# Kernel tuning notes

Measured on AMD Instinct MI355X. Metric: run time of the kernel, lower is better.

Reference implementation:

```python
import jax, jax.numpy as jnp
import numpy as np

B, NQ, NP = 4, 8192, 2048
DIM_INP, DIM, HID, OUT, NBLK = 256, 200, 128, 3, 5
VAR = 0.2 ** 2


def setup_inputs() -> dict:
    key = jax.random.key(0)
    ks = jax.random.split(key, 12)
    s = 0.05  # weight scale to keep activations sane
    return {
        "xyz_q": jax.random.uniform(ks[0], (B, NQ, 3), jnp.float32),
        "anchors": jax.random.uniform(ks[1], (B, NP, 3), jnp.float32),
        "anchor_feats": jax.random.normal(ks[2], (B, NP, DIM_INP), jnp.float32),
        "fc0_w": jax.random.normal(ks[3], (DIM_INP, DIM), jnp.float32) * s,
        "fc0_b": jnp.zeros((DIM,), jnp.float32),
        "fc1_w": jax.random.normal(ks[4], (DIM, HID), jnp.float32) * s,
        "fc1_b": jnp.zeros((HID,), jnp.float32),
        "blk_w0": jax.random.normal(ks[5], (NBLK, HID, HID), jnp.float32) * s,
        "blk_b0": jnp.zeros((NBLK, HID), jnp.float32),
        "blk_w1": jax.random.normal(ks[6], (NBLK, HID, HID), jnp.float32) * s,
        "blk_b1": jnp.zeros((NBLK, HID), jnp.float32),
        "fcc_w": jax.random.normal(ks[7], (NBLK, DIM, HID), jnp.float32) * s,
        "fcc_b": jnp.zeros((NBLK, HID), jnp.float32),
        "out_w": jax.random.normal(ks[8], (HID, OUT), jnp.float32) * s,
        "out_b": jnp.zeros((OUT,), jnp.float32),
    }


def reference(xyz_q, anchors, anchor_feats, fc0_w, fc0_b, fc1_w, fc1_b,
              blk_w0, blk_b0, blk_w1, blk_b1, fcc_w, fcc_b, out_w, out_b):
    relu = jax.nn.relu
    # Gaussian-kernel interpolation of anchor features at query points.
    # diff: [B, nq, np, 3]
    diff = anchors[:, None, :, :] - xyz_q[:, :, None, :]
    d = jnp.linalg.norm(diff, axis=-1)                    # [B, nq, np]
    logits = -((d + 1e-5) ** 2) / VAR
    weight = jax.nn.softmax(logits, axis=2)               # exp / sum, stable
    c = jnp.einsum('bqp,bpd->bqd', weight, anchor_feats)  # [B, nq, dim_inp]
    lat = c @ fc0_w + fc0_b                               # [B, nq, dim]
    net = relu(lat) @ fc1_w + fc1_b                       # [B, nq, hid]
    for i in range(NBLK):
        net = net + lat @ fcc_w[i] + fcc_b[i]
        # ResnetBlockFC: x + fc_1(relu(fc_0(relu(x))))
        dx = relu(relu(net) @ blk_w0[i] + blk_b0[i]) @ blk_w1[i] + blk_b1[i]
        net = net + dx
    return relu(net) @ out_w + out_b                      # [B, nq, 3]
```

## Files before the change

### kernel.cpp

```cpp
#include <hip/hip_runtime.h>
#include <math.h>

#define NP     2048
#define NQTOT  8192
#define DIN    256
#define DIM    200
#define HID    128
#define NOUT3  3
#define NBLK   5
#define TQ     32
#define NTHR   256
#define INVVAR 25.0f
#define NKT    (NP / 32)
#define NDT    (DIN / 16)
#define WSCALE 32768.0f
#define NFRAG  760

using f16x8 = __attribute__((ext_vector_type(8))) _Float16;
using f32x4 = __attribute__((ext_vector_type(4))) float;

__device__ __forceinline__ unsigned int pkrtz_u32(float a, float b) {
  auto p = __builtin_amdgcn_cvt_pkrtz(a, b);
  return __builtin_bit_cast(unsigned int, p);
}
__device__ __forceinline__ void pack_f16_2(const float* f, f16x8& h, f16x8& l) {
#pragma unroll
  for (int j = 0; j < 8; ++j) {
    const float v = f[j];
    const _Float16 hh = (_Float16)v;
    h[j] = hh; l[j] = (_Float16)(v - (float)hh);
  }
}
__device__ __forceinline__ void pack_w16(const float* f, f16x8& h, f16x8& l) {
#pragma unroll
  for (int j = 0; j < 8; ++j) {
    const float v = f[j] * WSCALE;
    const _Float16 hh = (_Float16)v;
    h[j] = hh; l[j] = (_Float16)(v - (float)hh);
  }
}
__device__ __forceinline__ void pack_a(const float* f, f16x8& h, f16x8& l) {
  union { f16x8 v; unsigned int u[4]; } H, L;
#pragma unroll
  for (int jp = 0; jp < 4; ++jp) {
    const float a = f[2 * jp], b = f[2 * jp + 1];
    auto hp = __builtin_amdgcn_cvt_pkrtz(a, b);
    H.u[jp] = __builtin_bit_cast(unsigned int, hp);
    L.u[jp] = pkrtz_u32(a - (float)hp[0], b - (float)hp[1]);
  }
  h = H.v; l = L.v;
}
__device__ __forceinline__ unsigned int split_pack(float x) {
  auto hp = __builtin_amdgcn_cvt_pkrtz(x, x);
  return pkrtz_u32(x, x - (float)hp[0]);
}

__device__ __forceinline__ int qsw(int r, int q) {
  return r * TQ + (q ^ (((r >> 2) & 7) << 2));
}
template<int KPAD>
__device__ __forceinline__ int sidx(int q, int k) {
  return q * KPAD + (((k >> 2) ^ (q & 7)) << 2) + (k & 3);
}

template<int KPAD, bool RELU>
__device__ __forceinline__ void store_split4(unsigned int* dst, int k, int qbase, f32x4 v) {
#pragma unroll
  for (int r = 0; r < 4; ++r) {
    float x = v[r];
    if (RELU) x = fmaxf(x, 0.f);
    dst[sidx<KPAD>(qbase + r, k)] = split_pack(x);
  }
}

__global__ __launch_bounds__(NTHR) void pid_packf(const float* __restrict__ F,
                                                  f16x8* __restrict__ wsHi,
                                                  f16x8* __restrict__ wsLo) {
  const int wid = threadIdx.x >> 6, l = threadIdx.x & 63;
  const int tile = blockIdx.x * 4 + wid;
  const int b  = tile >> 10;
  const int kt = (tile >> 4) & 63;
  const int dt = tile & 15;
  const int grp = l >> 4, qn = l & 15;
  const float* src = F + ((size_t)b * NP + kt * 32 + grp * 8) * DIN + dt * 16 + qn;
  float v[8];
#pragma unroll
  for (int j = 0; j < 8; ++j) v[j] = src[(size_t)j * DIN];
  f16x8 h, lo;
  pack_f16_2(v, h, lo);
  const size_t fi = (size_t)tile * 64 + l;
  wsHi[fi] = h; wsLo[fi] = lo;
}

__global__ __launch_bounds__(NTHR) void pid_packw(
    const float* __restrict__ fc0_w, const float* __restrict__ fc1_w,
    const float* __restrict__ fcc_w, const float* __restrict__ blk_w0,
    const float* __restrict__ blk_w1,
    f16x8* __restrict__ Wh, f16x8* __restrict__ Wm) {
  const int wid = threadIdx.x >> 6, l = threadIdx.x & 63;
  const int f = blockIdx.x * 4 + wid;
  if (f >= NFRAG) return;
  const float* src; int Kl, Nl, ks, nt;
  if (f < 104)      { int r = f;       src = fc0_w; Kl = 256; Nl = 200; ks = r / 13; nt = r % 13; }
  else if (f < 160) { int r = f - 104; src = fc1_w; Kl = 200; Nl = 128; ks = r / 8;  nt = r % 8; }
  else if (f < 440) { int r = f - 160; int i = r / 56; r %= 56;
                      src = fcc_w + (size_t)i * DIM * HID; Kl = 200; Nl = 128; ks = r / 8; nt = r % 8; }
  else if (f < 600) { int r = f - 440; int i = r / 32; r %= 32;
                      src = blk_w0 + (size_t)i * HID * HID; Kl = 128; Nl = 128; ks = r / 8; nt = r % 8; }
  else              { int r = f - 600; int i = r / 32; r %= 32;
                      src = blk_w1 + (size_t)i * HID * HID; Kl = 128; Nl = 128; ks = r / 8; nt = r % 8; }
  const int grp = l >> 4, n = nt * 16 + (l & 15);
  f16x8 h, m;
#pragma unroll
  for (int j = 0; j < 8; ++j) {
    const int k = ks * 32 + grp * 8 + j;
    const float v = (k < Kl && n < Nl) ? src[(size_t)k * Nl + n] : 0.f;
    const _Float16 hh = (_Float16)v;
    h[j] = hh; m[j] = (_Float16)(v - (float)hh);
  }
  const size_t fi = (size_t)f * 64 + l;
  Wh[fi] = h; Wm[fi] = m;
}

template<int KS, int NT, int MAXNT, int KPADIN, bool RELUA>
__device__ __forceinline__ void mm_stage(
    const unsigned int* __restrict__ Xs,
    const f16x8* __restrict__ Wh, const f16x8* __restrict__ Wm, int fbase,
    f32x4 acc[2][MAXNT], int wid, int l) {
  const int grp = l >> 4, qn = l & 15;
#pragma unroll 1
  for (int ks = 0; ks < KS; ++ks) {
    f16x8 bh[MAXNT], bm[MAXNT];
#pragma unroll
    for (int i = 0; i < MAXNT; ++i) {
      const int nt = wid + i * 4;
      if (nt < NT) {
        const size_t fi = (size_t)(fbase + ks * NT + nt) * 64 + l;
        bh[i] = Wh[fi]; bm[i] = Wm[fi];
      }
    }
    const int u0 = ks * 8 + grp * 2;
    f16x8 ah[2], al[2];
#pragma unroll
    for (int qt = 0; qt < 2; ++qt) {
      const int q = qt * 16 + qn;
      const unsigned int* row = Xs + q * KPADIN;
      const uint4 lo = *(const uint4*)(row + (((u0) ^ (q & 7)) << 2));
      const uint4 hi = *(const uint4*)(row + (((u0 + 1) ^ (q & 7)) << 2));
      unsigned int p[8] = {lo.x, lo.y, lo.z, lo.w, hi.x, hi.y, hi.z, hi.w};
      if (RELUA) {
#pragma unroll
        for (int j = 0; j < 8; ++j) p[j] = (p[j] & 0x8000u) ? 0u : p[j];
      }
      union { f16x8 v; unsigned int u[4]; } H, L;
#pragma unroll
      for (int jp = 0; jp < 4; ++jp) {
        H.u[jp] = __builtin_amdgcn_perm(p[2 * jp + 1], p[2 * jp], 0x05040100u);
        L.u[jp] = __builtin_amdgcn_perm(p[2 * jp + 1], p[2 * jp], 0x07060302u);
      }
      ah[qt] = H.v; al[qt] = L.v;
    }
#pragma unroll
    for (int qt = 0; qt < 2; ++qt)
#pragma unroll
      for (int i = 0; i < MAXNT; ++i)
        if (wid + i * 4 < NT) {
          acc[qt][i] = __builtin_amdgcn_mfma_f32_16x16x32_f16(ah[qt], bh[i], acc[qt][i], 0, 0, 0);
          acc[qt][i] = __builtin_amdgcn_mfma_f32_16x16x32_f16(ah[qt], bm[i], acc[qt][i], 0, 0, 0);
          acc[qt][i] = __builtin_amdgcn_mfma_f32_16x16x32_f16(al[qt], bh[i], acc[qt][i], 0, 0, 0);
        }
  }
}

struct SMemV2 {
  union {
    struct { float ax[NP * 3]; float qx[TQ], qy[TQ], qz[TQ]; } a;
    unsigned int lats[32 * 224];
  } r1;
  union {
    unsigned int cTs[32 * 256];
    struct { unsigned int nets[32 * 128]; unsigned int tmps[32 * 128]; } nt;
    float netf[128 * 32];
  } r2;
  float sS[64];
};

__global__ __launch_bounds__(NTHR, 2) void pid_fused_mfma(
    const float* __restrict__ xyz_q, const float* __restrict__ anchors,
    const f16x8* __restrict__ wsFh, const f16x8* __restrict__ wsFl,
    const f16x8* __restrict__ Wh, const f16x8* __restrict__ Wm,
    const float* __restrict__ fc0_b, const float* __restrict__ fc1_b,
    const float* __restrict__ blk_b0, const float* __restrict__ blk_b1,
    const float* __restrict__ fcc_b,
    const float* __restrict__ out_w, const float* __restrict__ out_b,
    float* __restrict__ out) {
  __shared__ SMemV2 sm;
  const int t = threadIdx.x;
  const int bi = blockIdx.x;
  const int batch = bi & 3;
  const int q0 = (bi >> 2) * TQ;

  {
    const float4* src = (const float4*)(anchors + (size_t)batch * NP * 3);
    float4* dst = (float4*)sm.r1.a.ax;
#pragma unroll
    for (int j = 0; j < (NP * 3 / 4) / NTHR; ++j)
      dst[j * NTHR + t] = src[j * NTHR + t];
  }
  if (t < TQ) {
    const float* qp = xyz_q + ((size_t)batch * NQTOT + q0 + t) * 3;
    sm.r1.a.qx[t] = qp[0]; sm.r1.a.qy[t] = qp[1]; sm.r1.a.qz[t] = qp[2];
  }
  __syncthreads();

  const int wid = t >> 6, l = t & 63;
  const int qt = wid & 1;
  const int kh = wid >> 1;
  const int grp = l >> 4, qn = l & 15;
  const float qxv = sm.r1.a.qx[qt * 16 + qn];
  const float qyv = sm.r1.a.qy[qt * 16 + qn];
  const float qzv = sm.r1.a.qz[qt * 16 + qn];
  const float nC1 = -36.067376f;
  const float nC2 = -7.2134752e-4f;

  const size_t fb0 = (size_t)batch * (NKT * NDT * 64) + (size_t)(kh * 32) * (NDT * 64) + l;
  const f16x8* pH0 = wsFh + fb0;        const f16x8* pL0 = wsFl + fb0;
  const f16x8* pH1 = pH0 + 256;         const f16x8* pL1 = pL0 + 256;
  const f16x8* pH2 = pH0 + 512;         const f16x8* pL2 = pL0 + 512;
  const f16x8* pH3 = pH0 + 768;         const f16x8* pL3 = pL0 + 768;

  f32x4 acc[16];
#pragma unroll
  for (int j = 0; j < 16; ++j) acc[j] = (f32x4){0.f, 0.f, 0.f, 0.f};
  float ssum = 0.f;

#pragma unroll 1
  for (int kt = 0; kt < 32; ++kt) {
    const int pb = (kh * 32 + kt) * 32 + grp * 8;
    float4 av[6];
    {
      const float4* ap = (const float4*)&sm.r1.a.ax[pb * 3];
#pragma unroll
      for (int j = 0; j < 6; ++j) av[j] = ap[j];
    }
    const float* af = (const float*)av;
    float w8[8];
#pragma unroll
    for (int j = 0; j < 8; ++j) {
      const float dx = af[3 * j] - qxv, dy = af[3 * j + 1] - qyv, dz = af[3 * j + 2] - qzv;
      const float D = fmaf(dx, dx, fmaf(dy, dy, dz * dz));
      const float s = __builtin_amdgcn_sqrtf(D);
      const float arg = fmaf(nC2, s, fmaf(nC1, D, 15.0f));
      const float u = __builtin_amdgcn_exp2f(arg);
      w8[j] = u; ssum += u;
    }
    f16x8 ah, al;
    pack_a(w8, ah, al);
#define CHUNK(dc, PH, PL)                                                     \
    {                                                                         \
      f16x8 bh[4], bl[4];                                                     \
      _Pragma("unroll") for (int k = 0; k < 4; ++k) {                         \
        bh[k] = PH[k * 64]; bl[k] = PL[k * 64];                               \
      }                                                                       \
      _Pragma("unroll") for (int k = 0; k < 4; ++k) {                         \
        f32x4 a = acc[dc * 4 + k];                                            \
        a = __builtin_amdgcn_mfma_f32_16x16x32_f16(ah, bh[k], a, 0, 0, 0);    \
        a = __builtin_amdgcn_mfma_f32_16x16x32_f16(ah, bl[k], a, 0, 0, 0);    \
        a = __builtin_amdgcn_mfma_f32_16x16x32_f16(al, bh[k], a, 0, 0, 0);    \
        acc[dc * 4 + k] = a;                                                  \
      }                                                                       \
    }
    CHUNK(0, pH0, pL0) CHUNK(1, pH1, pL1) CHUNK(2, pH2, pL2) CHUNK(3, pH3, pL3)
#undef CHUNK
    pH0 += 1024; pH1 += 1024; pH2 += 1024; pH3 += 1024;
    pL0 += 1024; pL1 += 1024; pL2 += 1024; pL3 += 1024;
  }

  ssum += __shfl_xor(ssum, 16);
  ssum += __shfl_xor(ssum, 32);
  if ((l & 48) == 0) sm.sS[kh * 32 + qt * 16 + qn] = ssum;

  float4* P = (float4*)sm.r2.cTs;
  if (kh == 0) {
#pragma unroll
    for (int dt = 0; dt < 16; ++dt)
      P[(qt * 16 + dt) * 64 + grp * 16 + qn] =
          make_float4(acc[dt][0], acc[dt][1], acc[dt][2], acc[dt][3]);
  }
  __syncthreads();
  if (kh == 1) {
#pragma unroll
    for (int dt = 0; dt < 16; ++dt) {
      const float4 pv = P[(qt * 16 + dt) * 64 + grp * 16 + qn];
      acc[dt][0] += pv.x; acc[dt][1] += pv.y; acc[dt][2] += pv.z; acc[dt][3] += pv.w;
    }
    float sc[4];
#pragma unroll
    for (int r = 0; r < 4; ++r) {
      const int q = qt * 16 + grp * 4 + r;
      sc[r] = __builtin_amdgcn_rcpf(sm.sS[q] + sm.sS[32 + q]);
    }
#pragma unroll
    for (int dt = 0; dt < 16; ++dt) {
      const f32x4 v = {acc[dt][0] * sc[0], acc[dt][1] * sc[1],
                       acc[dt][2] * sc[2], acc[dt][3] * sc[3]};
      store_split4<256, false>(sm.r2.cTs, dt * 16 + qn, qt * 16 + grp * 4, v);
    }
  } else {
#pragma unroll
    for (int z = 0; z < 6; ++z) {
      const int idx = t * 6 + z;
      const int q = idx / 24, kk = 200 + idx % 24;
      sm.r1.lats[sidx<224>(q, kk)] = 0u;
    }
  }
  __syncthreads();

  {
    f32x4 a0[2][4];
#pragma unroll
    for (int i = 0; i < 4; ++i) {
      const int nt = wid + i * 4;
      if (nt < 13) {
        const int n = nt * 16 + qn;
        const float b = (n < 200) ? fc0_b[n] : 0.f;
#pragma unroll
        for (int q2 = 0; q2 < 2; ++q2) a0[q2][i] = (f32x4){b, b, b, b};
      }
    }
    mm_stage<8, 13, 4, 256, false>(sm.r2.cTs, Wh, Wm, 0, a0, wid, l);
#pragma unroll
    for (int q2 = 0; q2 < 2; ++q2)
#pragma unroll
      for (int i = 0; i < 4; ++i) {
        const int nt = wid + i * 4;
        if (nt < 13)
          store_split4<224, false>(sm.r1.lats, nt * 16 + qn, q2 * 16 + grp * 4, a0[q2][i]);
      }
  }
  __syncthreads();

  f32x4 net[2][2];
#pragma unroll
  for (int i = 0; i < 2; ++i) {
    const float b = fc1_b[(wid + i * 4) * 16 + qn];
#pragma unroll
    for (int q2 = 0; q2 < 2; ++q2) net[q2][i] = (f32x4){b, b, b, b};
  }
  mm_stage<7, 8, 2, 224, true>(sm.r1.lats, Wh, Wm, 104, net, wid, l);

#pragma unroll 1
  for (int ib = 0; ib < NBLK; ++ib) {
#pragma unroll
    for (int i = 0; i < 2; ++i) {
      const float b = fcc_b[ib * HID + (wid + i * 4) * 16 + qn];
#pragma unroll
      for (int q2 = 0; q2 < 2; ++q2) net[q2][i] += (f32x4){b, b, b, b};
    }
    mm_stage<7, 8, 2, 224, false>(sm.r1.lats, Wh, Wm, 160 + 56 * ib, net, wid, l);
#pragma unroll
    for (int q2 = 0; q2 < 2; ++q2)
#pragma unroll
      for (int i = 0; i < 2; ++i)
        store_split4<128, true>(sm.r2.nt.nets, (wid + i * 4) * 16 + qn,
                                q2 * 16 + grp * 4, net[q2][i]);
    __syncthreads();
    f32x4 a2[2][2];
#pragma unroll
    for (int i = 0; i < 2; ++i) {
      const float b = blk_b0[ib * HID + (wid + i * 4) * 16 + qn];
#pragma unroll
      for (int q2 = 0; q2 < 2; ++q2) a2[q2][i] = (f32x4){b, b, b, b};
    }
    mm_stage<4, 8, 2, 128, false>(sm.r2.nt.nets, Wh, Wm, 440 + 32 * ib, a2, wid, l);
#pragma unroll
    for (int q2 = 0; q2 < 2; ++q2)
#pragma unroll
      for (int i = 0; i < 2; ++i)
        store_split4<128, true>(sm.r2.nt.tmps, (wid + i * 4) * 16 + qn,
                                q2 * 16 + grp * 4, a2[q2][i]);
    __syncthreads();
#pragma unroll
    for (int i = 0; i < 2; ++i) {
      const float b = blk_b1[ib * HID + (wid + i * 4) * 16 + qn];
#pragma unroll
      for (int q2 = 0; q2 < 2; ++q2) net[q2][i] += (f32x4){b, b, b, b};
    }
    mm_stage<4, 8, 2, 128, false>(sm.r2.nt.tmps, Wh, Wm, 600 + 32 * ib, net, wid, l);
    __syncthreads();
  }

#pragma unroll
  for (int q2 = 0; q2 < 2; ++q2)
#pragma unroll
    for (int i = 0; i < 2; ++i) {
      const int n = (wid + i * 4) * 16 + qn;
      *(float4*)&sm.r2.netf[n * 32 + q2 * 16 + grp * 4] =
          make_float4(net[q2][i][0], net[q2][i][1], net[q2][i][2], net[q2][i][3]);
    }
  __syncthreads();
  if (t < TQ * NOUT3) {
    const int q = t / NOUT3, n = t - q * NOUT3;
    float s = out_b[n];
#pragma unroll 8
    for (int k = 0; k < HID; ++k)
      s = fmaf(fmaxf(sm.r2.netf[k * 32 + q], 0.f), out_w[k * NOUT3 + n], s);
    out[((size_t)batch * NQTOT + q0 + q) * NOUT3 + n] = s;
  }
}

template<int K, bool RELUX, bool ACCY>
__device__ __forceinline__ void stage_h128(const float* __restrict__ X,
                                           const float* __restrict__ Wg,
                                           const float* __restrict__ bg,
                                           float* __restrict__ Y, int t) {
  const int qg = t & 7, ng = t >> 3;
  const int n0 = ng * 4, q0 = qg * 4;
  const float4 bv = *(const float4*)&bg[n0];
  const float br[4] = {bv.x, bv.y, bv.z, bv.w};
  float acc[4][4];
#pragma unroll
  for (int j = 0; j < 4; ++j) {
    if (ACCY) {
      const float4 yv = *(const float4*)&Y[qsw(n0 + j, q0)];
      acc[0][j] = yv.x + br[j]; acc[1][j] = yv.y + br[j];
      acc[2][j] = yv.z + br[j]; acc[3][j] = yv.w + br[j];
    } else {
      acc[0][j] = br[j]; acc[1][j] = br[j]; acc[2][j] = br[j]; acc[3][j] = br[j];
    }
  }
#pragma unroll 2
  for (int k0 = 0; k0 < K; k0 += 8) {
    float4 wr[8];
#pragma unroll
    for (int kk = 0; kk < 8; ++kk)
      wr[kk] = *(const float4*)&Wg[(size_t)(k0 + kk) * HID + n0];
#pragma unroll
    for (int kk = 0; kk < 8; ++kk) {
      float4 xv = *(const float4*)&X[qsw(k0 + kk, q0)];
      if (RELUX) {
        xv.x = fmaxf(xv.x, 0.f); xv.y = fmaxf(xv.y, 0.f);
        xv.z = fmaxf(xv.z, 0.f); xv.w = fmaxf(xv.w, 0.f);
      }
      const float xr[4] = {xv.x, xv.y, xv.z, xv.w};
      const float wl[4] = {wr[kk].x, wr[kk].y, wr[kk].z, wr[kk].w};
#pragma unroll
      for (int i = 0; i < 4; ++i)
#pragma unroll
        for (int j = 0; j < 4; ++j)
          acc[i][j] = fmaf(xr[i], wl[j], acc[i][j]);
    }
  }
#pragma unroll
  for (int j = 0; j < 4; ++j)
    *(float4*)&Y[qsw(n0 + j, q0)] =
        make_float4(acc[0][j], acc[1][j], acc[2][j], acc[3][j]);
}

__device__ __forceinline__ void stage_fc0v(const float* __restrict__ X,
                                           const float* __restrict__ Wg,
                                           const float* __restrict__ bg,
                                           float* __restrict__ Y, int t) {
  const int qg = t & 7, ng = t >> 3;
  const int n0 = ng * 8, q0 = qg * 4;
  const bool act = (ng < 25);
  float acc[4][8];
  if (act) {
    const float4 b0 = *(const float4*)&bg[n0];
    const float4 b1 = *(const float4*)&bg[n0 + 4];
    const float br[8] = {b0.x, b0.y, b0.z, b0.w, b1.x, b1.y, b1.z, b1.w};
#pragma unroll
    for (int j = 0; j < 8; ++j)
#pragma unroll
      for (int i = 0; i < 4; ++i) acc[i][j] = br[j];
  }
#pragma unroll 2
  for (int k0 = 0; k0 < DIN; k0 += 4) {
    if (act) {
      float4 wa[4], wb[4];
#pragma unroll
      for (int kk = 0; kk < 4; ++kk) {
        wa[kk] = *(const float4*)&Wg[(size_t)(k0 + kk) * DIM + n0];
        wb[kk] = *(const float4*)&Wg[(size_t)(k0 + kk) * DIM + n0 + 4];
      }
#pragma unroll
      for (int kk = 0; kk < 4; ++kk) {
        const float4 xv = *(const float4*)&X[qsw(k0 + kk, q0)];
        const float xr[4] = {xv.x, xv.y, xv.z, xv.w};
        const float wl[8] = {wa[kk].x, wa[kk].y, wa[kk].z, wa[kk].w,
                             wb[kk].x, wb[kk].y, wb[kk].z, wb[kk].w};
#pragma unroll
        for (int i = 0; i < 4; ++i)
#pragma unroll
          for (int j = 0; j < 8; ++j)
            acc[i][j] = fmaf(xr[i], wl[j], acc[i][j]);
      }
    }
  }
  if (act) {
#pragma unroll
    for (int j = 0; j < 8; ++j)
      *(float4*)&Y[qsw(n0 + j, q0)] =
          make_float4(acc[0][j], acc[1][j], acc[2][j], acc[3][j]);
  }
}

struct SA1 {
  float ax[NP * 3];
  float qx[TQ], qy[TQ], qz[TQ], m[TQ];
  float sred[8 * TQ];
};
struct SB1 {
  float lat[DIM * TQ];
  union {
    float cT[DIN * TQ];
    struct { float net[HID * TQ]; float tmp[HID * TQ]; } nt;
  } u;
};
struct SMem1 { union { SA1 a; SB1 b; } s; float sS[TQ]; };

__global__ __launch_bounds__(NTHR, 2) void pid_fused_vec(
    const float* __restrict__ xyz_q, const float* __restrict__ anchors,
    const f16x8* __restrict__ wsFh, const f16x8* __restrict__ wsFl,
    const float* __restrict__ fc0_w, const float* __restrict__ fc0_b,
    const float* __restrict__ fc1_w, const float* __restrict__ fc1_b,
    const float* __restrict__ blk_w0, const float* __restrict__ blk_b0,
    const float* __restrict__ blk_w1, const float* __restrict__ blk_b1,
    const float* __restrict__ fcc_w, const float* __restrict__ fcc_b,
    const float* __restrict__ out_w, const float* __restrict__ out_b,
    float* __restrict__ out) {
  __shared__ SMem1 sm;
  const int t = threadIdx.x;
  const int bi = blockIdx.x;
  const int batch = bi & 3;
  const int q0 = (bi >> 2) * TQ;

  {
    const float4* src = (const float4*)(anchors + (size_t)batch * NP * 3);
    float4* dst = (float4*)sm.s.a.ax;
#pragma unroll
    for (int j = 0; j < (NP * 3 / 4) / NTHR; ++j)
      dst[j * NTHR + t] = src[j * NTHR + t];
  }
  if (t < TQ) {
    const float* qp = xyz_q + ((size_t)batch * NQTOT + q0 + t) * 3;
    sm.s.a.qx[t] = qp[0]; sm.s.a.qy[t] = qp[1]; sm.s.a.qz[t] = qp[2];
  }
  __syncthreads();
  {
    const int q = t & 31, g = t >> 5;
    const float qxv = sm.s.a.qx[q], qyv = sm.s.a.qy[q], qzv = sm.s.a.qz[q];
    float mloc = 3.0e38f;
    const float* az = sm.s.a.ax + g * 256 * 3;
    for (int pi = 0; pi < 256; ++pi) {
      const float dx = az[pi * 3 + 0] - qxv;
      const float dy = az[pi * 3 + 1] - qyv;
      const float dz = az[pi * 3 + 2] - qzv;
      mloc = fminf(mloc, fmaf(dx, dx, fmaf(dy, dy, dz * dz)));
    }
    sm.s.a.sred[g * TQ + q] = mloc;
  }
  __syncthreads();
  if (t < TQ) {
    float mv = sm.s.a.sred[t];
#pragma unroll
    for (int g = 1; g < 8; ++g) mv = fminf(mv, sm.s.a.sred[g * TQ + t]);
    const float dmin = sqrtf(mv) + 1e-5f;
    sm.s.a.m[t] = -dmin * dmin * INVVAR;
  }
  __syncthreads();

  const int wid = t >> 6, l = t & 63;
  const int qt = wid & 1;
  const int dgb = (wid >> 1) * 8;
  const int grp = l >> 4, qn = l & 15;
  const float qxv = sm.s.a.qx[qt * 16 + qn];
  const float qyv = sm.s.a.qy[qt * 16 + qn];
  const float qzv = sm.s.a.qz[qt * 16 + qn];
  const float negm = -sm.s.a.m[qt * 16 + qn];
  const f16x8* BH = wsFh + (size_t)batch * NKT * NDT * 64;
  const f16x8* BL = wsFl + (size_t)batch * NKT * NDT * 64;

  f32x4 acc[8];
#pragma unroll
  for (int j = 0; j < 8; ++j) acc[j] = (f32x4){0.f, 0.f, 0.f, 0.f};
  float ssum = 0.f;
#pragma unroll 1
  for (int kt = 0; kt < NKT; ++kt) {
    f16x8 bh[8], bl[8];
#pragma unroll
    for (int d2 = 0; d2 < 8; ++d2) {
      const size_t fi = ((size_t)kt * NDT + dgb + d2) * 64 + l;
      bh[d2] = BH[fi]; bl[d2] = BL[fi];
    }
    const int pb = kt * 32 + grp * 8;
    float4 av[6];
    {
      const float4* ap = (const float4*)&sm.s.a.ax[pb * 3];
#pragma unroll
      for (int j = 0; j < 6; ++j) av[j] = ap[j];
    }
    const float* af = (const float*)av;
    float w8[8];
#pragma unroll
    for (int j = 0; j < 8; ++j) {
      const float dx = af[3 * j] - qxv, dy = af[3 * j + 1] - qyv, dz = af[3 * j + 2] - qzv;
      const float d = sqrtf(fmaf(dx, dx, fmaf(dy, dy, dz * dz))) + 1e-5f;
      const float u = __expf(fmaf(d * d, -INVVAR, negm));
      w8[j] = u; ssum += u;
    }
    f16x8 ah, al;
    pack_w16(w8, ah, al);
#pragma unroll
    for (int d2 = 0; d2 < 8; ++d2)
      acc[d2] = __builtin_amdgcn_mfma_f32_16x16x32_f16(ah, bh[d2], acc[d2], 0, 0, 0);
#pragma unroll
    for (int d2 = 0; d2 < 8; ++d2)
      acc[d2] = __builtin_amdgcn_mfma_f32_16x16x32_f16(ah, bl[d2], acc[d2], 0, 0, 0);
#pragma unroll
    for (int d2 = 0; d2 < 8; ++d2)
      acc[d2] = __builtin_amdgcn_mfma_f32_16x16x32_f16(al, bh[d2], acc[d2], 0, 0, 0);
  }
  ssum += __shfl_xor(ssum, 16);
  ssum += __shfl_xor(ssum, 32);
  if (wid < 2 && grp == 0) sm.sS[qt * 16 + qn] = ssum;
  __syncthreads();
  float sc[4];
#pragma unroll
  for (int r = 0; r < 4; ++r)
    sc[r] = (1.0f / WSCALE) / sm.sS[qt * 16 + grp * 4 + r];
#pragma unroll
  for (int d2 = 0; d2 < 8; ++d2) {
    const int d = (dgb + d2) * 16 + qn;
    *(float4*)&sm.s.b.u.cT[qsw(d, qt * 16 + grp * 4)] =
        make_float4(acc[d2][0] * sc[0], acc[d2][1] * sc[1],
                    acc[d2][2] * sc[2], acc[d2][3] * sc[3]);
  }
  __syncthreads();

  stage_fc0v(sm.s.b.u.cT, fc0_w, fc0_b, sm.s.b.lat, t);
  __syncthreads();
  stage_h128<DIM, true, false>(sm.s.b.lat, fc1_w, fc1_b, sm.s.b.u.nt.net, t);
  __syncthreads();
#pragma unroll 1
  for (int i = 0; i < NBLK; ++i) {
    stage_h128<DIM, false, true>(sm.s.b.lat, fcc_w + (size_t)i * DIM * HID,
                                 fcc_b + i * HID, sm.s.b.u.nt.net, t);
    __syncthreads();
    stage_h128<HID, true, false>(sm.s.b.u.nt.net, blk_w0 + (size_t)i * HID * HID,
                                 blk_b0 + i * HID, sm.s.b.u.nt.tmp, t);
    __syncthreads();
    stage_h128<HID, true, true>(sm.s.b.u.nt.tmp, blk_w1 + (size_t)i * HID * HID,
                                blk_b1 + i * HID, sm.s.b.u.nt.net, t);
    __syncthreads();
  }
  if (t < TQ * NOUT3) {
    const int q = t / NOUT3, n = t - q * NOUT3;
    float s = out_b[n];
    const float* net = sm.s.b.u.nt.net;
#pragma unroll 8
    for (int k = 0; k < HID; ++k)
      s = fmaf(fmaxf(net[k * TQ + (q ^ (((k >> 2) & 7) << 2))], 0.f),
               out_w[k * NOUT3 + n], s);
    out[((size_t)batch * NQTOT + q0 + q) * NOUT3 + n] = s;
  }
}

extern "C" void kernel_launch(void* const* d_in, const int* in_sizes, int n_in,
                              void* d_out, int out_size, void* d_ws, size_t ws_size,
                              hipStream_t stream) {
  (void)in_sizes; (void)n_in; (void)out_size;
  const float* xyz_q        = (const float*)d_in[0];
  const float* anchors      = (const float*)d_in[1];
  const float* anchor_feats = (const float*)d_in[2];
  const float* fc0_w        = (const float*)d_in[3];
  const float* fc0_b        = (const float*)d_in[4];
  const float* fc1_w        = (const float*)d_in[5];
  const float* fc1_b        = (const float*)d_in[6];
  const float* blk_w0       = (const float*)d_in[7];
  const float* blk_b0       = (const float*)d_in[8];
  const float* blk_w1       = (const float*)d_in[9];
  const float* blk_b1       = (const float*)d_in[10];
  const float* fcc_w        = (const float*)d_in[11];
  const float* fcc_b        = (const float*)d_in[12];
  const float* out_w        = (const float*)d_in[13];
  const float* out_b        = (const float*)d_in[14];
  float* out = (float*)d_out;

  const size_t F_BYTES = (size_t)4 * NKT * NDT * 64 * 16;
  const size_t W_BYTES = (size_t)NFRAG * 64 * 16;
  f16x8* wsFh = (f16x8*)d_ws;
  f16x8* wsFl = (f16x8*)((char*)d_ws + F_BYTES);
  f16x8* Wh   = (f16x8*)((char*)d_ws + 2 * F_BYTES);
  f16x8* Wm   = (f16x8*)((char*)d_ws + 2 * F_BYTES + W_BYTES);

  hipLaunchKernelGGL(pid_packf, dim3(1024), dim3(NTHR), 0, stream,
                     anchor_feats, wsFh, wsFl);
  if (ws_size >= 2 * F_BYTES + 2 * W_BYTES) {
    hipLaunchKernelGGL(pid_packw, dim3((NFRAG + 3) / 4), dim3(NTHR), 0, stream,
                       fc0_w, fc1_w, fcc_w, blk_w0, blk_w1, Wh, Wm);
    hipLaunchKernelGGL(pid_fused_mfma, dim3(1024), dim3(NTHR), 0, stream,
                       xyz_q, anchors, wsFh, wsFl, Wh, Wm,
                       fc0_b, fc1_b, blk_b0, blk_b1, fcc_b, out_w, out_b, out);
  } else {
    hipLaunchKernelGGL(pid_fused_vec, dim3(1024), dim3(NTHR), 0, stream,
                       xyz_q, anchors, wsFh, wsFl,
                       fc0_w, fc0_b, fc1_w, fc1_b, blk_w0, blk_b0,
                       blk_w1, blk_b1, fcc_w, fcc_b, out_w, out_b, out);
  }
}
```

Before: 278.5 us.

## Stage anchor-feature tiles in LDS and split output dims across waves

New measurement: 671.0 us. 2.41x slower.

```diff
diff --git a/kernel.cpp b/kernel.cpp
--- a/kernel.cpp
+++ b/kernel.cpp
@@ -178,6 +178,7 @@
     unsigned int lats[32 * 224];
   } r1;
   union {
+    uint4 stage[2048];
     unsigned int cTs[32 * 256];
     struct { unsigned int nets[32 * 128]; unsigned int tmps[32 * 128]; } nt;
     float netf[128 * 32];
@@ -215,7 +216,7 @@
 
   const int wid = t >> 6, l = t & 63;
   const int qt = wid & 1;
-  const int kh = wid >> 1;
+  const int dh = wid >> 1;
   const int grp = l >> 4, qn = l & 15;
   const float qxv = sm.r1.a.qx[qt * 16 + qn];
   const float qyv = sm.r1.a.qy[qt * 16 + qn];
@@ -223,20 +224,43 @@
   const float nC1 = -36.067376f;
   const float nC2 = -7.2134752e-4f;
 
-  const size_t fb0 = (size_t)batch * (NKT * NDT * 64) + (size_t)(kh * 32) * (NDT * 64) + l;
-  const f16x8* pH0 = wsFh + fb0;        const f16x8* pL0 = wsFl + fb0;
-  const f16x8* pH1 = pH0 + 256;         const f16x8* pL1 = pL0 + 256;
-  const f16x8* pH2 = pH0 + 512;         const f16x8* pL2 = pL0 + 512;
-  const f16x8* pH3 = pH0 + 768;         const f16x8* pL3 = pL0 + 768;
-
-  f32x4 acc[16];
-#pragma unroll
-  for (int j = 0; j < 16; ++j) acc[j] = (f32x4){0.f, 0.f, 0.f, 0.f};
+  const uint4* __restrict__ srcH =
+      (const uint4*)(wsFh + (size_t)batch * (NKT * NDT * 64));
+  const uint4* __restrict__ srcL =
+      (const uint4*)(wsFl + (size_t)batch * (NKT * NDT * 64));
+  uint4* const Bs = sm.r2.stage;
+
+  f32x4 acc[8];
+#pragma unroll
+  for (int j = 0; j < 8; ++j) acc[j] = (f32x4){0.f, 0.f, 0.f, 0.f};
   float ssum = 0.f;
 
+  uint4 pf[8];
+#pragma unroll
+  for (int i = 0; i < 4; ++i) {
+    pf[i]     = srcH[t + 256 * i];
+    pf[4 + i] = srcL[t + 256 * i];
+  }
+
 #pragma unroll 1
-  for (int kt = 0; kt < 32; ++kt) {
-    const int pb = (kh * 32 + kt) * 32 + grp * 8;
+  for (int kt = 0; kt < NKT; ++kt) {
+    __syncthreads();
+#pragma unroll
+    for (int i = 0; i < 4; ++i) {
+      Bs[t + 256 * i]        = pf[i];
+      Bs[1024 + t + 256 * i] = pf[4 + i];
+    }
+    if (kt + 1 < NKT) {
+      const int o = (kt + 1) * 1024;
+#pragma unroll
+      for (int i = 0; i < 4; ++i) {
+        pf[i]     = srcH[o + t + 256 * i];
+        pf[4 + i] = srcL[o + t + 256 * i];
+      }
+    }
+    __syncthreads();
+
+    const int pb = kt * 32 + grp * 8;
     float4 av[6];
     {
       const float4* ap = (const float4*)&sm.r1.a.ax[pb * 3];
@@ -256,60 +280,39 @@
     }
     f16x8 ah, al;
     pack_a(w8, ah, al);
-#define CHUNK(dc, PH, PL)                                                     \
-    {                                                                         \
-      f16x8 bh[4], bl[4];                                                     \
-      _Pragma("unroll") for (int k = 0; k < 4; ++k) {                         \
-        bh[k] = PH[k * 64]; bl[k] = PL[k * 64];                               \
-      }                                                                       \
-      _Pragma("unroll") for (int k = 0; k < 4; ++k) {                         \
-        f32x4 a = acc[dc * 4 + k];                                            \
-        a = __builtin_amdgcn_mfma_f32_16x16x32_f16(ah, bh[k], a, 0, 0, 0);    \
-        a = __builtin_amdgcn_mfma_f32_16x16x32_f16(ah, bl[k], a, 0, 0, 0);    \
-        a = __builtin_amdgcn_mfma_f32_16x16x32_f16(al, bh[k], a, 0, 0, 0);    \
-        acc[dc * 4 + k] = a;                                                  \
-      }                                                                       \
-    }
-    CHUNK(0, pH0, pL0) CHUNK(1, pH1, pL1) CHUNK(2, pH2, pL2) CHUNK(3, pH3, pL3)
-#undef CHUNK
-    pH0 += 1024; pH1 += 1024; pH2 += 1024; pH3 += 1024;
-    pL0 += 1024; pL1 += 1024; pL2 += 1024; pL3 += 1024;
-  }
+
+#pragma unroll
+    for (int d2 = 0; d2 < 8; ++d2) {
+      const int dt = dh * 8 + d2;
+      const f16x8 bh = __builtin_bit_cast(f16x8, Bs[dt * 64 + l]);
+      const f16x8 bl = __builtin_bit_cast(f16x8, Bs[1024 + dt * 64 + l]);
+      f32x4 a = acc[d2];
+      a = __builtin_amdgcn_mfma_f32_16x16x32_f16(ah, bh, a, 0, 0, 0);
+      a = __builtin_amdgcn_mfma_f32_16x16x32_f16(ah, bl, a, 0, 0, 0);
+      a = __builtin_amdgcn_mfma_f32_16x16x32_f16(al, bh, a, 0, 0, 0);
+      acc[d2] = a;
+    }
+  }
+  __syncthreads();
 
   ssum += __shfl_xor(ssum, 16);
   ssum += __shfl_xor(ssum, 32);
-  if ((l & 48) == 0) sm.sS[kh * 32 + qt * 16 + qn] = ssum;
-
-  float4* P = (float4*)sm.r2.cTs;
-  if (kh == 0) {
-#pragma unroll
-    for (int dt = 0; dt < 16; ++dt)
-      P[(qt * 16 + dt) * 64 + grp * 16 + qn] =
-          make_float4(acc[dt][0], acc[dt][1], acc[dt][2], acc[dt][3]);
-  }
-  __syncthreads();
-  if (kh == 1) {
-#pragma unroll
-    for (int dt = 0; dt < 16; ++dt) {
-      const float4 pv = P[(qt * 16 + dt) * 64 + grp * 16 + qn];
-      acc[dt][0] += pv.x; acc[dt][1] += pv.y; acc[dt][2] += pv.z; acc[dt][3] += pv.w;
-    }
-    float sc[4];
-#pragma unroll
-    for (int r = 0; r < 4; ++r) {
-      const int q = qt * 16 + grp * 4 + r;
-      sc[r] = __builtin_amdgcn_rcpf(sm.sS[q] + sm.sS[32 + q]);
-    }
-#pragma unroll
-    for (int dt = 0; dt < 16; ++dt) {
-      const f32x4 v = {acc[dt][0] * sc[0], acc[dt][1] * sc[1],
-                       acc[dt][2] * sc[2], acc[dt][3] * sc[3]};
-      store_split4<256, false>(sm.r2.cTs, dt * 16 + qn, qt * 16 + grp * 4, v);
-    }
-  } else {
-#pragma unroll
-    for (int z = 0; z < 6; ++z) {
-      const int idx = t * 6 + z;
+  float sc[4];
+#pragma unroll
+  for (int r = 0; r < 4; ++r)
+    sc[r] = __builtin_amdgcn_rcpf(__shfl(ssum, grp * 4 + r));
+
+#pragma unroll
+  for (int d2 = 0; d2 < 8; ++d2) {
+    const int k = (dh * 8 + d2) * 16 + qn;
+    const f32x4 v = {acc[d2][0] * sc[0], acc[d2][1] * sc[1],
+                     acc[d2][2] * sc[2], acc[d2][3] * sc[3]};
+    store_split4<256, false>(sm.r2.cTs, k, qt * 16 + grp * 4, v);
+  }
+  {
+#pragma unroll
+    for (int z = 0; z < 3; ++z) {
+      const int idx = t * 3 + z;
       const int q = idx / 24, kk = 200 + idx % 24;
       sm.r1.lats[sidx<224>(q, kk)] = 0u;
     }
```

## Repartition interpolation waves to share B-fragment loads across both query tiles

Applied to the files above, without the earlier changes.

After: 262.4 us. 1.06x faster.

```diff
diff --git a/kernel.cpp b/kernel.cpp
--- a/kernel.cpp
+++ b/kernel.cpp
@@ -214,29 +214,28 @@
   __syncthreads();
 
   const int wid = t >> 6, l = t & 63;
-  const int qt = wid & 1;
-  const int kh = wid >> 1;
+  const int kp = wid & 1;
+  const int dh = wid >> 1;
   const int grp = l >> 4, qn = l & 15;
-  const float qxv = sm.r1.a.qx[qt * 16 + qn];
-  const float qyv = sm.r1.a.qy[qt * 16 + qn];
-  const float qzv = sm.r1.a.qz[qt * 16 + qn];
+  const float q0x = sm.r1.a.qx[qn],      q0y = sm.r1.a.qy[qn],      q0z = sm.r1.a.qz[qn];
+  const float q1x = sm.r1.a.qx[16 + qn], q1y = sm.r1.a.qy[16 + qn], q1z = sm.r1.a.qz[16 + qn];
   const float nC1 = -36.067376f;
   const float nC2 = -7.2134752e-4f;
 
-  const size_t fb0 = (size_t)batch * (NKT * NDT * 64) + (size_t)(kh * 32) * (NDT * 64) + l;
-  const f16x8* pH0 = wsFh + fb0;        const f16x8* pL0 = wsFl + fb0;
-  const f16x8* pH1 = pH0 + 256;         const f16x8* pL1 = pL0 + 256;
-  const f16x8* pH2 = pH0 + 512;         const f16x8* pL2 = pL0 + 512;
-  const f16x8* pH3 = pH0 + 768;         const f16x8* pL3 = pL0 + 768;
-
-  f32x4 acc[16];
-#pragma unroll
-  for (int j = 0; j < 16; ++j) acc[j] = (f32x4){0.f, 0.f, 0.f, 0.f};
-  float ssum = 0.f;
+  const size_t fb = (size_t)batch * (NKT * NDT * 64) + kp * 1024 + dh * 512 + l;
+  const f16x8* pH0 = wsFh + fb;  const f16x8* pL0 = wsFl + fb;
+  const f16x8* pH1 = pH0 + 256;  const f16x8* pL1 = pL0 + 256;
+
+  f32x4 acc[2][8];
+#pragma unroll
+  for (int a = 0; a < 2; ++a)
+#pragma unroll
+    for (int j = 0; j < 8; ++j) acc[a][j] = (f32x4){0.f, 0.f, 0.f, 0.f};
+  float s0 = 0.f, s1 = 0.f;
 
 #pragma unroll 1
-  for (int kt = 0; kt < 32; ++kt) {
-    const int pb = (kh * 32 + kt) * 32 + grp * 8;
+  for (int kt = kp; kt < NKT; kt += 2) {
+    const int pb = kt * 32 + grp * 8;
     float4 av[6];
     {
       const float4* ap = (const float4*)&sm.r1.a.ax[pb * 3];
@@ -247,71 +246,103 @@
     float w8[8];
 #pragma unroll
     for (int j = 0; j < 8; ++j) {
-      const float dx = af[3 * j] - qxv, dy = af[3 * j + 1] - qyv, dz = af[3 * j + 2] - qzv;
+      const float dx = af[3 * j] - q0x, dy = af[3 * j + 1] - q0y, dz = af[3 * j + 2] - q0z;
       const float D = fmaf(dx, dx, fmaf(dy, dy, dz * dz));
       const float s = __builtin_amdgcn_sqrtf(D);
-      const float arg = fmaf(nC2, s, fmaf(nC1, D, 15.0f));
-      const float u = __builtin_amdgcn_exp2f(arg);
-      w8[j] = u; ssum += u;
-    }
-    f16x8 ah, al;
-    pack_a(w8, ah, al);
-#define CHUNK(dc, PH, PL)                                                     \
+      const float u = __builtin_amdgcn_exp2f(fmaf(nC2, s, fmaf(nC1, D, 15.0f)));
+      w8[j] = u; s0 += u;
+    }
+    f16x8 ah0, al0;
+    pack_a(w8, ah0, al0);
+#pragma unroll
+    for (int j = 0; j < 8; ++j) {
+      const float dx = af[3 * j] - q1x, dy = af[3 * j + 1] - q1y, dz = af[3 * j + 2] - q1z;
+      const float D = fmaf(dx, dx, fmaf(dy, dy, dz * dz));
+      const float s = __builtin_amdgcn_sqrtf(D);
+      const float u = __builtin_amdgcn_exp2f(fmaf(nC2, s, fmaf(nC1, D, 15.0f)));
+      w8[j] = u; s1 += u;
+    }
+    f16x8 ah1, al1;
+    pack_a(w8, ah1, al1);
+
+#define CHUNK2(PH, PL, DOFF)                                                  \
     {                                                                         \
       f16x8 bh[4], bl[4];                                                     \
       _Pragma("unroll") for (int k = 0; k < 4; ++k) {                         \
         bh[k] = PH[k * 64]; bl[k] = PL[k * 64];                               \
       }                                                                       \
       _Pragma("unroll") for (int k = 0; k < 4; ++k) {                         \
-        f32x4 a = acc[dc * 4 + k];                                            \
-        a = __builtin_amdgcn_mfma_f32_16x16x32_f16(ah, bh[k], a, 0, 0, 0);    \
-        a = __builtin_amdgcn_mfma_f32_16x16x32_f16(ah, bl[k], a, 0, 0, 0);    \
-        a = __builtin_amdgcn_mfma_f32_16x16x32_f16(al, bh[k], a, 0, 0, 0);    \
-        acc[dc * 4 + k] = a;                                                  \
+        f32x4 a0 = acc[0][DOFF + k];                                          \
+        a0 = __builtin_amdgcn_mfma_f32_16x16x32_f16(ah0, bh[k], a0, 0, 0, 0); \
+        a0 = __builtin_amdgcn_mfma_f32_16x16x32_f16(ah0, bl[k], a0, 0, 0, 0); \
+        a0 = __builtin_amdgcn_mfma_f32_16x16x32_f16(al0, bh[k], a0, 0, 0, 0); \
+        acc[0][DOFF + k] = a0;                                                \
+        f32x4 a1 = acc[1][DOFF + k];                                          \
+        a1 = __builtin_amdgcn_mfma_f32_16x16x32_f16(ah1, bh[k], a1, 0, 0, 0); \
+        a1 = __builtin_amdgcn_mfma_f32_16x16x32_f16(ah1, bl[k], a1, 0, 0, 0); \
+        a1 = __builtin_amdgcn_mfma_f32_16x16x32_f16(al1, bh[k], a1, 0, 0, 0); \
+        acc[1][DOFF + k] = a1;                                                \
       }                                                                       \
     }
-    CHUNK(0, pH0, pL0) CHUNK(1, pH1, pL1) CHUNK(2, pH2, pL2) CHUNK(3, pH3, pL3)
-#undef CHUNK
-    pH0 += 1024; pH1 += 1024; pH2 += 1024; pH3 += 1024;
-    pL0 += 1024; pL1 += 1024; pL2 += 1024; pL3 += 1024;
-  }
-
-  ssum += __shfl_xor(ssum, 16);
-  ssum += __shfl_xor(ssum, 32);
-  if ((l & 48) == 0) sm.sS[kh * 32 + qt * 16 + qn] = ssum;
-
+    CHUNK2(pH0, pL0, 0)
+    CHUNK2(pH1, pL1, 4)
+#undef CHUNK2
+    pH0 += 2048; pL0 += 2048; pH1 += 2048; pL1 += 2048;
+  }
+
+  s0 += __shfl_xor(s0, 16); s0 += __shfl_xor(s0, 32);
+  s1 += __shfl_xor(s1, 16); s1 += __shfl_xor(s1, 32);
+  if (dh == 0 && l < 16) {
+    sm.sS[kp * 32 + qn] = s0;
+    sm.sS[kp * 32 + 16 + qn] = s1;
+  }
   float4* P = (float4*)sm.r2.cTs;
-  if (kh == 0) {
-#pragma unroll
-    for (int dt = 0; dt < 16; ++dt)
-      P[(qt * 16 + dt) * 64 + grp * 16 + qn] =
-          make_float4(acc[dt][0], acc[dt][1], acc[dt][2], acc[dt][3]);
-  }
-  __syncthreads();
-  if (kh == 1) {
-#pragma unroll
-    for (int dt = 0; dt < 16; ++dt) {
-      const float4 pv = P[(qt * 16 + dt) * 64 + grp * 16 + qn];
-      acc[dt][0] += pv.x; acc[dt][1] += pv.y; acc[dt][2] += pv.z; acc[dt][3] += pv.w;
-    }
-    float sc[4];
-#pragma unroll
-    for (int r = 0; r < 4; ++r) {
-      const int q = qt * 16 + grp * 4 + r;
-      sc[r] = __builtin_amdgcn_rcpf(sm.sS[q] + sm.sS[32 + q]);
-    }
-#pragma unroll
-    for (int dt = 0; dt < 16; ++dt) {
-      const f32x4 v = {acc[dt][0] * sc[0], acc[dt][1] * sc[1],
-                       acc[dt][2] * sc[2], acc[dt][3] * sc[3]};
-      store_split4<256, false>(sm.r2.cTs, dt * 16 + qn, qt * 16 + grp * 4, v);
-    }
+  if (kp == 0) {
+#pragma unroll
+    for (int qt2 = 0; qt2 < 2; ++qt2)
+#pragma unroll
+      for (int d2 = 0; d2 < 8; ++d2)
+        P[(qt2 * 16 + dh * 8 + d2) * 64 + grp * 16 + qn] =
+            make_float4(acc[qt2][d2][0], acc[qt2][d2][1],
+                        acc[qt2][d2][2], acc[qt2][d2][3]);
+  }
+  __syncthreads();
+  if (kp == 1) {
+#pragma unroll
+    for (int qt2 = 0; qt2 < 2; ++qt2)
+#pragma unroll
+      for (int d2 = 0; d2 < 8; ++d2) {
+        const float4 pv = P[(qt2 * 16 + dh * 8 + d2) * 64 + grp * 16 + qn];
+        acc[qt2][d2][0] += pv.x; acc[qt2][d2][1] += pv.y;
+        acc[qt2][d2][2] += pv.z; acc[qt2][d2][3] += pv.w;
+      }
   } else {
+    const int lid = (wid >> 1) * 64 + l;
 #pragma unroll
     for (int z = 0; z < 6; ++z) {
-      const int idx = t * 6 + z;
+      const int idx = lid * 6 + z;
       const int q = idx / 24, kk = 200 + idx % 24;
       sm.r1.lats[sidx<224>(q, kk)] = 0u;
+    }
+  }
+  __syncthreads();
+  if (kp == 1) {
+    float sc0[4], sc1[4];
+#pragma unroll
+    for (int r = 0; r < 4; ++r) {
+      const int j = grp * 4 + r;
+      sc0[r] = __builtin_amdgcn_rcpf(sm.sS[j] + sm.sS[32 + j]);
+      sc1[r] = __builtin_amdgcn_rcpf(sm.sS[16 + j] + sm.sS[48 + j]);
+    }
+#pragma unroll
+    for (int d2 = 0; d2 < 8; ++d2) {
+      const int k = (dh * 8 + d2) * 16 + qn;
+      const f32x4 v0 = {acc[0][d2][0] * sc0[0], acc[0][d2][1] * sc0[1],
+                        acc[0][d2][2] * sc0[2], acc[0][d2][3] * sc0[3]};
+      store_split4<256, false>(sm.r2.cTs, k, grp * 4, v0);
+      const f32x4 v1 = {acc[1][d2][0] * sc1[0], acc[1][d2][1] * sc1[1],
+                        acc[1][d2][2] * sc1[2], acc[1][d2][3] * sc1[3]};
+      store_split4<256, false>(sm.r2.cTs, k, 16 + grp * 4, v1);
     }
   }
   __syncthreads();
```
